# Performance work log

Hardware: AMD Instinct MI355X
Metric: run time of the kernel (lower is better)

Reference implementation:

```python
import jax, jax.numpy as jnp
import numpy as np

N_NODES = 50000
N_EDGES = 800000
IN_DIM, H1, H2 = 512, 128, 64


def setup_inputs() -> dict:
    key = jax.random.key(0)
    k1, k2, k3, k4 = jax.random.split(key, 4)
    x = jax.random.normal(k1, (N_NODES, IN_DIM), dtype=jnp.float32)
    edge_index = jax.random.randint(k2, (2, N_EDGES), 0, N_NODES, dtype=jnp.int64)
    # Glorot-ish scaled weights (PyG GCNConv uses glorot init)
    W1 = jax.random.normal(k3, (IN_DIM, H1), dtype=jnp.float32) * (1.0 / np.sqrt(IN_DIM))
    b1 = jnp.zeros((H1,), dtype=jnp.float32)
    W2 = jax.random.normal(k4, (H1, H2), dtype=jnp.float32) * (1.0 / np.sqrt(H1))
    b2 = jnp.zeros((H2,), dtype=jnp.float32)
    return {"x": x, "edge_index": edge_index, "W1": W1, "b1": b1, "W2": W2, "b2": b2}


def reference(x, edge_index, W1, b1, W2, b2):
    N = x.shape[0]
    # PyG GCNConv default: add self-loops + symmetric normalization
    loop = jnp.arange(N, dtype=edge_index.dtype)
    src = jnp.concatenate([edge_index[0], loop])  # message source j
    dst = jnp.concatenate([edge_index[1], loop])  # aggregation target i
    deg = jax.ops.segment_sum(jnp.ones(src.shape[0], dtype=x.dtype), dst, num_segments=N)
    dinv = jnp.where(deg > 0, jax.lax.rsqrt(deg), 0.0)
    norm = dinv[src] * dinv[dst]  # [E+N]

    def gcn_relu(h, W, b):
        h = h @ W                                   # [N, F_out]
        msg = h[src] * norm[:, None]                # gather + edge scaling
        agg = jax.ops.segment_sum(msg, dst, num_segments=N)  # scatter-add
        return jax.nn.relu(agg + b)

    h = gcn_relu(x, W1, b1)
    return gcn_relu(h, W2, b2)
```

## Files before the change

kernel.cpp:

```cpp
#include <hip/hip_runtime.h>


constexpr int IN_DIM = 512;
constexpr int HD1 = 128;
constexpr int HD2 = 64;

typedef __attribute__((ext_vector_type(8))) short bf16x8;
typedef __attribute__((ext_vector_type(8))) unsigned short u16x8;
typedef __attribute__((ext_vector_type(4))) float f32x4;
typedef unsigned int u32;

__device__ inline unsigned short f2bf(float f) {
    u32 u = __builtin_bit_cast(u32, f);
    return (unsigned short)((u + 0x7fffu + ((u >> 16) & 1u)) >> 16);
}
__device__ inline float bf_lo(u32 v) { return __builtin_bit_cast(float, v << 16); }
__device__ inline float bf_hi(u32 v) { return __builtin_bit_cast(float, v & 0xffff0000u); }

__device__ inline int elem_off(int row, int k) {
    return (row << 6) + (k ^ ((row & 7) << 3));
}
__device__ inline int elem_off128(int row, int k) {
    return (row << 7) + (k ^ ((row & 7) << 3));
}

__global__ __launch_bounds__(256) void k_prep(const int* __restrict__ dst, int E,
                                              int* __restrict__ deg,
                                              int* __restrict__ rank,
                                              const float* __restrict__ W1,
                                              unsigned short* __restrict__ Wt,
                                              const float* __restrict__ W2,
                                              unsigned short* __restrict__ Wt2) {
    int id = blockIdx.x * 256 + threadIdx.x;
    if (id < E) rank[id] = atomicAdd(&deg[dst[id]], 1);
    if (id < IN_DIM * HD1) {
        int n = id >> 9, k = id & 511;
        Wt[id] = f2bf(W1[k * HD1 + n]);
    }
    if (id < HD1 * HD2) {
        int n = id >> 7, k = id & 127;
        Wt2[id] = f2bf(W2[k * HD2 + n]);
    }
}

__global__ __launch_bounds__(256) void k_dinv_bsum(const int* __restrict__ deg, int N,
                                                   float* __restrict__ dinv,
                                                   int* __restrict__ bsum) {
    __shared__ int s[256];
    int t = threadIdx.x;
    int i = blockIdx.x * 256 + t;
    int d = (i < N) ? deg[i] : 0;
    if (i < N) dinv[i] = rsqrtf((float)(d + 1));
    s[t] = d;
    __syncthreads();
    for (int st = 128; st > 0; st >>= 1) {
        if (t < st) s[t] += s[t + st];
        __syncthreads();
    }
    if (t == 0) bsum[blockIdx.x] = s[0];
}

__global__ __launch_bounds__(256) void k_scan_final(const int* __restrict__ deg, int N,
                                                    const int* __restrict__ bsum, int nb,
                                                    int* __restrict__ rowptr) {
    __shared__ int sb[256];
    __shared__ int s[256];
    int t = threadIdx.x;
    sb[t] = (t < nb) ? bsum[t] : 0;
    __syncthreads();
    for (int off = 1; off < 256; off <<= 1) {
        int v = (t >= off) ? sb[t - off] : 0;
        __syncthreads();
        sb[t] += v;
        __syncthreads();
    }
    int base = (blockIdx.x == 0) ? 0 : sb[blockIdx.x - 1];

    int i = blockIdx.x * 256 + t;
    int v = (i < N) ? deg[i] : 0;
    s[t] = v;
    __syncthreads();
    for (int off = 1; off < 256; off <<= 1) {
        int u = (t >= off) ? s[t - off] : 0;
        __syncthreads();
        s[t] += u;
        __syncthreads();
    }
    int incl = s[t] + base;
    if (i < N) rowptr[i] = incl - v;
    if (i == N - 1) rowptr[N] = incl;
}

__global__ __launch_bounds__(256) void k_mega(const float* __restrict__ X,
                                              const unsigned short* __restrict__ Wt,
                                              unsigned short* __restrict__ H, int N,
                                              int gemmBlocks,
                                              const int* __restrict__ src,
                                              const int* __restrict__ dst, int E,
                                              const int* __restrict__ rowptr,
                                              const int* __restrict__ rank,
                                              int* __restrict__ col) {
    __shared__ unsigned short As[128 * 64];
    __shared__ unsigned short Bs[128 * 64];

    if (blockIdx.x >= gemmBlocks) {
        int stride = (gridDim.x - gemmBlocks) * 256;
        for (int e = (blockIdx.x - gemmBlocks) * 256 + threadIdx.x; e < E; e += stride) {
            int d = dst[e];
            col[rowptr[d] + rank[e]] = src[e];
        }
        return;
    }

    const int tid = threadIdx.x;
    const int lane = tid & 63;
    const int wid = tid >> 6;
    const int brow = blockIdx.x * 128;
    const int wr0 = (wid >> 1) * 64;
    const int wc0 = (wid & 1) * 64;
    const bool full = (brow + 128 <= N);

    f32x4 acc[4][4];
#pragma unroll
    for (int i = 0; i < 4; i++)
#pragma unroll
        for (int j = 0; j < 4; j++) acc[i][j] = (f32x4){0.f, 0.f, 0.f, 0.f};

    for (int kt = 0; kt < IN_DIM / 64; kt++) {
        const int k0 = kt * 64;
#pragma unroll
        for (int p = 0; p < 4; p++) {
            int chunk = (wid * 4 + p) * 64 + lane;
            int n = chunk >> 3;
            int kcs = chunk & 7;
            int kc = kcs ^ (n & 7);
            const unsigned short* srcp = &Wt[(size_t)n * IN_DIM + k0 + kc * 8];
            unsigned short* dstp = &Bs[(wid * 4 + p) * 512];
            __builtin_amdgcn_global_load_lds(
                (const __attribute__((address_space(1))) u32*)(const void*)srcp,
                (__attribute__((address_space(3))) u32*)(void*)dstp, 16, 0, 0);
        }
#pragma unroll
        for (int p = 0; p < 4; p++) {
            int chunk = tid + p * 256;
            int r = chunk >> 3;
            int kc = chunk & 7;
            const float* xp = &X[(size_t)(brow + r) * IN_DIM + k0 + kc * 8];
            float4 v0, v1;
            if (full || (brow + r) < N) {
                v0 = *(const float4*)xp;
                v1 = *(const float4*)(xp + 4);
            } else {
                v0 = make_float4(0.f, 0.f, 0.f, 0.f); v1 = v0;
            }
            u16x8 w;
            w[0] = f2bf(v0.x); w[1] = f2bf(v0.y); w[2] = f2bf(v0.z); w[3] = f2bf(v0.w);
            w[4] = f2bf(v1.x); w[5] = f2bf(v1.y); w[6] = f2bf(v1.z); w[7] = f2bf(v1.w);
            *(u16x8*)&As[elem_off(r, kc * 8)] = w;
        }
        __syncthreads();

#pragma unroll
        for (int kk = 0; kk < 2; kk++) {
            const int kel = kk * 32 + (lane >> 4) * 8;
            bf16x8 a[4], b[4];
#pragma unroll
            for (int mi = 0; mi < 4; mi++)
                a[mi] = *(const bf16x8*)&As[elem_off(wr0 + mi * 16 + (lane & 15), kel)];
#pragma unroll
            for (int ni = 0; ni < 4; ni++)
                b[ni] = *(const bf16x8*)&Bs[elem_off(wc0 + ni * 16 + (lane & 15), kel)];
#pragma unroll
            for (int mi = 0; mi < 4; mi++)
#pragma unroll
                for (int ni = 0; ni < 4; ni++)
                    acc[mi][ni] = __builtin_amdgcn_mfma_f32_16x16x32_bf16(
                        a[mi], b[ni], acc[mi][ni], 0, 0, 0);
        }
        __syncthreads();
    }

#pragma unroll
    for (int mi = 0; mi < 4; mi++) {
#pragma unroll
        for (int reg = 0; reg < 4; reg++) {
            int grow = brow + wr0 + mi * 16 + (lane >> 4) * 4 + reg;
            if (grow < N) {
#pragma unroll
                for (int ni = 0; ni < 4; ni++) {
                    int gcol = wc0 + ni * 16 + (lane & 15);
                    H[(size_t)grow * HD1 + gcol] = f2bf(acc[mi][ni][reg]);
                }
            }
        }
    }
}

__global__ __launch_bounds__(256) void k_gather1(const unsigned short* __restrict__ h,
                                                 const int* __restrict__ rowptr,
                                                 const int* __restrict__ col,
                                                 const float* __restrict__ dinv,
                                                 const float* __restrict__ bias,
                                                 unsigned short* __restrict__ out, int N) {
    const int i = (blockIdx.x * 256 + threadIdx.x) >> 6;
    const int lane = threadIdx.x & 63;
    if (i >= N) return;
    const int half = lane >> 5;
    const int c4 = (lane & 31) * 4;
    const float di = dinv[i];
    const unsigned short* hc = h + c4;

    float a0 = 0.f, a1 = 0.f, a2 = 0.f, a3 = 0.f;
    if (half == 0) {
        uint2 sv = *(const uint2*)&hc[(size_t)i * HD1];
        float s = di * di;
        a0 = bf_lo(sv.x) * s; a1 = bf_hi(sv.x) * s;
        a2 = bf_lo(sv.y) * s; a3 = bf_hi(sv.y) * s;
    }
    const int beg = rowptr[i], end = rowptr[i + 1];
    for (int p0 = beg; p0 < end; p0 += 64) {
        int idx = p0 + lane;
        bool okl = idx < end;
        int myj = okl ? col[idx] : i;
        float mydj = okl ? dinv[myj] : 0.f;
        const int cnt8 = (min(64, end - p0) + 7) & ~7;
        uint2 v[4]; float wv[4];
#pragma unroll
        for (int q = 0; q < 4; q++) {
            int e = 2 * q + half;
            int j = __shfl(myj, e);
            wv[q] = __shfl(mydj, e) * di;
            v[q] = *(const uint2*)&hc[(size_t)j * HD1];
        }
        for (int k = 8; k < cnt8; k += 8) {
            uint2 nv[4]; float nw[4];
#pragma unroll
            for (int q = 0; q < 4; q++) {
                int e = k + 2 * q + half;
                int j = __shfl(myj, e);
                nw[q] = __shfl(mydj, e) * di;
                nv[q] = *(const uint2*)&hc[(size_t)j * HD1];
            }
#pragma unroll
            for (int q = 0; q < 4; q++) {
                a0 = fmaf(bf_lo(v[q].x), wv[q], a0);
                a1 = fmaf(bf_hi(v[q].x), wv[q], a1);
                a2 = fmaf(bf_lo(v[q].y), wv[q], a2);
                a3 = fmaf(bf_hi(v[q].y), wv[q], a3);
            }
#pragma unroll
            for (int q = 0; q < 4; q++) { v[q] = nv[q]; wv[q] = nw[q]; }
        }
#pragma unroll
        for (int q = 0; q < 4; q++) {
            a0 = fmaf(bf_lo(v[q].x), wv[q], a0);
            a1 = fmaf(bf_hi(v[q].x), wv[q], a1);
            a2 = fmaf(bf_lo(v[q].y), wv[q], a2);
            a3 = fmaf(bf_hi(v[q].y), wv[q], a3);
        }
    }
    a0 += __shfl_xor(a0, 32);
    a1 += __shfl_xor(a1, 32);
    a2 += __shfl_xor(a2, 32);
    a3 += __shfl_xor(a3, 32);
    if (half == 0) {
        float4 bv = *(const float4*)&bias[c4];
        u32 w0 = (u32)f2bf(fmaxf(a0 + bv.x, 0.f)) | ((u32)f2bf(fmaxf(a1 + bv.y, 0.f)) << 16);
        u32 w1 = (u32)f2bf(fmaxf(a2 + bv.z, 0.f)) | ((u32)f2bf(fmaxf(a3 + bv.w, 0.f)) << 16);
        *(uint2*)&out[(size_t)i * HD1 + c4] = make_uint2(w0, w1);
    }
}

__global__ __launch_bounds__(256) void k_gemm2(const unsigned short* __restrict__ A,
                                               const unsigned short* __restrict__ Wt2,
                                               unsigned short* __restrict__ H, int N) {
    __shared__ unsigned short As[128 * 128];
    __shared__ unsigned short Bs[64 * 128];
    const int tid = threadIdx.x;
    const int lane = tid & 63;
    const int wid = tid >> 6;
    const int brow = blockIdx.x * 128;
    const int wr0 = wid * 32;

#pragma unroll
    for (int p = 0; p < 8; p++) {
        int chunk = (wid * 8 + p) * 64 + lane;
        int r = chunk >> 4;
        int kcs = chunk & 15;
        int kc = kcs ^ (r & 7);
        const unsigned short* src = &A[(size_t)(brow + r) * HD1 + kc * 8];
        unsigned short* dst = &As[(wid * 8 + p) * 512];
        __builtin_amdgcn_global_load_lds(
            (const __attribute__((address_space(1))) u32*)(const void*)src,
            (__attribute__((address_space(3))) u32*)(void*)dst, 16, 0, 0);
    }
#pragma unroll
    for (int p = 0; p < 4; p++) {
        int chunk = (wid * 4 + p) * 64 + lane;
        int c = chunk >> 4;
        int kcs = chunk & 15;
        int kc = kcs ^ (c & 7);
        const unsigned short* src = &Wt2[(size_t)c * HD1 + kc * 8];
        unsigned short* dst = &Bs[(wid * 4 + p) * 512];
        __builtin_amdgcn_global_load_lds(
            (const __attribute__((address_space(1))) u32*)(const void*)src,
            (__attribute__((address_space(3))) u32*)(void*)dst, 16, 0, 0);
    }
    __syncthreads();

    f32x4 acc[2][4];
#pragma unroll
    for (int i = 0; i < 2; i++)
#pragma unroll
        for (int j = 0; j < 4; j++) acc[i][j] = (f32x4){0.f, 0.f, 0.f, 0.f};

#pragma unroll
    for (int kk = 0; kk < 4; kk++) {
        const int kel = kk * 32 + (lane >> 4) * 8;
        bf16x8 a[2], b[4];
#pragma unroll
        for (int mi = 0; mi < 2; mi++)
            a[mi] = *(const bf16x8*)&As[elem_off128(wr0 + mi * 16 + (lane & 15), kel)];
#pragma unroll
        for (int ni = 0; ni < 4; ni++)
            b[ni] = *(const bf16x8*)&Bs[elem_off128(ni * 16 + (lane & 15), kel)];
#pragma unroll
        for (int mi = 0; mi < 2; mi++)
#pragma unroll
            for (int ni = 0; ni < 4; ni++)
                acc[mi][ni] = __builtin_amdgcn_mfma_f32_16x16x32_bf16(
                    a[mi], b[ni], acc[mi][ni], 0, 0, 0);
    }

#pragma unroll
    for (int mi = 0; mi < 2; mi++) {
#pragma unroll
        for (int reg = 0; reg < 4; reg++) {
            int grow = brow + wr0 + mi * 16 + (lane >> 4) * 4 + reg;
            if (grow < N) {
#pragma unroll
                for (int ni = 0; ni < 4; ni++) {
                    int gcol = ni * 16 + (lane & 15);
                    H[(size_t)grow * HD2 + gcol] = f2bf(acc[mi][ni][reg]);
                }
            }
        }
    }
}

__global__ __launch_bounds__(256) void k_gather2(const unsigned short* __restrict__ h,
                                                 const int* __restrict__ rowptr,
                                                 const int* __restrict__ col,
                                                 const float* __restrict__ dinv,
                                                 const float* __restrict__ bias,
                                                 float* __restrict__ out, int N) {
    const int i = (blockIdx.x * 256 + threadIdx.x) >> 6;
    const int lane = threadIdx.x & 63;
    if (i >= N) return;
    const int half = lane >> 5;
    const int c2 = (lane & 31) * 2;
    const float di = dinv[i];
    const unsigned short* hc = h + c2;

    float a0 = 0.f, a1 = 0.f;
    if (half == 0) {
        u32 sv = *(const u32*)&hc[(size_t)i * HD2];
        float s = di * di;
        a0 = bf_lo(sv) * s; a1 = bf_hi(sv) * s;
    }
    const int beg = rowptr[i], end = rowptr[i + 1];
    for (int p0 = beg; p0 < end; p0 += 64) {
        int idx = p0 + lane;
        bool okl = idx < end;
        int myj = okl ? col[idx] : i;
        float mydj = okl ? dinv[myj] : 0.f;
        const int cnt8 = (min(64, end - p0) + 7) & ~7;
        u32 v[4]; float wv[4];
#pragma unroll
        for (int q = 0; q < 4; q++) {
            int e = 2 * q + half;
            int j = __shfl(myj, e);
            wv[q] = __shfl(mydj, e) * di;
            v[q] = *(const u32*)&hc[(size_t)j * HD2];
        }
        for (int k = 8; k < cnt8; k += 8) {
            u32 nv[4]; float nw[4];
#pragma unroll
            for (int q = 0; q < 4; q++) {
                int e = k + 2 * q + half;
                int j = __shfl(myj, e);
                nw[q] = __shfl(mydj, e) * di;
                nv[q] = *(const u32*)&hc[(size_t)j * HD2];
            }
#pragma unroll
            for (int q = 0; q < 4; q++) {
                a0 = fmaf(bf_lo(v[q]), wv[q], a0);
                a1 = fmaf(bf_hi(v[q]), wv[q], a1);
            }
#pragma unroll
            for (int q = 0; q < 4; q++) { v[q] = nv[q]; wv[q] = nw[q]; }
        }
#pragma unroll
        for (int q = 0; q < 4; q++) {
            a0 = fmaf(bf_lo(v[q]), wv[q], a0);
            a1 = fmaf(bf_hi(v[q]), wv[q], a1);
        }
    }
    a0 += __shfl_xor(a0, 32);
    a1 += __shfl_xor(a1, 32);
    if (half == 0) {
        float2 bv = *(const float2*)&bias[c2];
        float2 r = make_float2(fmaxf(a0 + bv.x, 0.f), fmaxf(a1 + bv.y, 0.f));
        *(float2*)&out[(size_t)i * HD2 + c2] = r;
    }
}

extern "C" void kernel_launch(void* const* d_in, const int* in_sizes, int n_in,
                              void* d_out, int out_size, void* d_ws, size_t ws_size,
                              hipStream_t stream) {
    const float* x  = (const float*)d_in[0];
    const int*   ei = (const int*)d_in[1];
    const float* W1 = (const float*)d_in[2];
    const float* b1 = (const float*)d_in[3];
    const float* W2 = (const float*)d_in[4];
    const float* b2 = (const float*)d_in[5];
    float* out = (float*)d_out;

    const int N = in_sizes[0] / IN_DIM;
    const int E = in_sizes[1] / 2;
    const int* src = ei;
    const int* dst = ei + E;

    char* w = (char*)d_ws;
    size_t off = 0;
    auto alloc = [&](size_t bytes) -> void* {
        void* p = w + off;
        off = (off + bytes + 255) & ~(size_t)255;
        return p;
    };
    int*   deg    = (int*)alloc((size_t)N * 4);
    int*   rank   = (int*)alloc((size_t)E * 4);
    int*   rowptr = (int*)alloc((size_t)(N + 1) * 4);
    int*   bsum   = (int*)alloc(1024 * 4);
    int*   col    = (int*)alloc((size_t)E * 4);
    float* dinv   = (float*)alloc((size_t)N * 4);
    unsigned short* Wt  = (unsigned short*)alloc((size_t)IN_DIM * HD1 * 2);
    unsigned short* Wt2 = (unsigned short*)alloc((size_t)HD2 * HD1 * 2);
    unsigned short* h1  = (unsigned short*)alloc((size_t)N * HD1 * 2);
    unsigned short* agg1= (unsigned short*)alloc((size_t)(N + 128) * HD1 * 2);
    unsigned short* h2  = h1;

    hipMemsetAsync(deg, 0, (size_t)N * 4, stream);

    const int nb = (N + 255) / 256;
    const int eb = (E + 255) / 256;
    const int gemmBlocks = (N + 127) / 128;
    const int fillBlocks = 512;

    k_prep<<<eb, 256, 0, stream>>>(dst, E, deg, rank, W1, Wt, W2, Wt2);
    k_dinv_bsum<<<nb, 256, 0, stream>>>(deg, N, dinv, bsum);
    k_scan_final<<<nb, 256, 0, stream>>>(deg, N, bsum, nb, rowptr);

    k_mega<<<gemmBlocks + fillBlocks, 256, 0, stream>>>(
        x, Wt, h1, N, gemmBlocks, src, dst, E, rowptr, rank, col);

    k_gather1<<<(N * 64 + 255) / 256, 256, 0, stream>>>(h1, rowptr, col, dinv, b1, agg1, N);
    k_gemm2<<<(N + 127) / 128, 256, 0, stream>>>(agg1, Wt2, h2, N);
    k_gather2<<<(N * 64 + 255) / 256, 256, 0, stream>>>(h2, rowptr, col, dinv, b2, out, N);
}
```

Before: 147.3 us.

## Load X directly into registers and double-buffer weight tiles in fused GEMM

The first GEMM stops staging X through shared memory. Each wave now loads its fp32 X rows straight from global memory, converts them to bf16 in registers and feeds them to MFMA. The weight tiles are double-buffered in LDS, with the next tile's async load issued before computing the current one, which removes one barrier per k-step. The CSR fill path batches four edges per thread with nontemporal stores, and the number of fill blocks doubles. The tradeoff is that each X element is now read by both column waves, so uncoalesced global traffic rises and there is more register pressure.

```diff
diff --git a/kernel.cpp b/kernel.cpp
--- a/kernel.cpp
+++ b/kernel.cpp
@@ -91,6 +91,22 @@
     if (i == N - 1) rowptr[N] = incl;
 }
 
+__device__ inline void issue_b_tile(const unsigned short* __restrict__ Wt, int k0,
+                                    unsigned short* bs, int wid, int lane) {
+#pragma unroll
+    for (int p = 0; p < 4; p++) {
+        int chunk = (wid * 4 + p) * 64 + lane;
+        int n = chunk >> 3;
+        int kcs = chunk & 7;
+        int kc = kcs ^ (n & 7);
+        const unsigned short* srcp = &Wt[(size_t)n * IN_DIM + k0 + kc * 8];
+        unsigned short* dstp = bs + (wid * 4 + p) * 512;
+        __builtin_amdgcn_global_load_lds(
+            (const __attribute__((address_space(1))) u32*)(const void*)srcp,
+            (__attribute__((address_space(3))) u32*)(void*)dstp, 16, 0, 0);
+    }
+}
+
 __global__ __launch_bounds__(256) void k_mega(const float* __restrict__ X,
                                               const unsigned short* __restrict__ Wt,
                                               unsigned short* __restrict__ H, int N,
@@ -100,12 +116,28 @@
                                               const int* __restrict__ rowptr,
                                               const int* __restrict__ rank,
                                               int* __restrict__ col) {
-    __shared__ unsigned short As[128 * 64];
-    __shared__ unsigned short Bs[128 * 64];
+    __shared__ unsigned short Bs[2][128 * 64];
 
     if (blockIdx.x >= gemmBlocks) {
-        int stride = (gridDim.x - gemmBlocks) * 256;
-        for (int e = (blockIdx.x - gemmBlocks) * 256 + threadIdx.x; e < E; e += stride) {
+        const int T = (gridDim.x - gemmBlocks) * 256;
+        const int e0 = (blockIdx.x - gemmBlocks) * 256 + threadIdx.x;
+        const int e1 = e0 + T, e2 = e1 + T, e3 = e2 + T;
+        const bool v0 = e0 < E, v1 = e1 < E, v2 = e2 < E, v3 = e3 < E;
+        int d0, d1, d2, d3, r0, r1, r2, r3, s0, s1, s2, s3;
+        if (v0) { d0 = dst[e0]; r0 = rank[e0]; s0 = src[e0]; }
+        if (v1) { d1 = dst[e1]; r1 = rank[e1]; s1 = src[e1]; }
+        if (v2) { d2 = dst[e2]; r2 = rank[e2]; s2 = src[e2]; }
+        if (v3) { d3 = dst[e3]; r3 = rank[e3]; s3 = src[e3]; }
+        int p0, p1, p2, p3;
+        if (v0) p0 = rowptr[d0] + r0;
+        if (v1) p1 = rowptr[d1] + r1;
+        if (v2) p2 = rowptr[d2] + r2;
+        if (v3) p3 = rowptr[d3] + r3;
+        if (v0) __builtin_nontemporal_store(s0, &col[p0]);
+        if (v1) __builtin_nontemporal_store(s1, &col[p1]);
+        if (v2) __builtin_nontemporal_store(s2, &col[p2]);
+        if (v3) __builtin_nontemporal_store(s3, &col[p3]);
+        for (int e = e0 + 4 * T; e < E; e += T) {
             int d = dst[e];
             col[rowptr[d] + rank[e]] = src[e];
         }
@@ -126,50 +158,36 @@
 #pragma unroll
         for (int j = 0; j < 4; j++) acc[i][j] = (f32x4){0.f, 0.f, 0.f, 0.f};
 
+    issue_b_tile(Wt, 0, &Bs[0][0], wid, lane);
+
     for (int kt = 0; kt < IN_DIM / 64; kt++) {
-        const int k0 = kt * 64;
-#pragma unroll
-        for (int p = 0; p < 4; p++) {
-            int chunk = (wid * 4 + p) * 64 + lane;
-            int n = chunk >> 3;
-            int kcs = chunk & 7;
-            int kc = kcs ^ (n & 7);
-            const unsigned short* srcp = &Wt[(size_t)n * IN_DIM + k0 + kc * 8];
-            unsigned short* dstp = &Bs[(wid * 4 + p) * 512];
-            __builtin_amdgcn_global_load_lds(
-                (const __attribute__((address_space(1))) u32*)(const void*)srcp,
-                (__attribute__((address_space(3))) u32*)(void*)dstp, 16, 0, 0);
-        }
-#pragma unroll
-        for (int p = 0; p < 4; p++) {
-            int chunk = tid + p * 256;
-            int r = chunk >> 3;
-            int kc = chunk & 7;
-            const float* xp = &X[(size_t)(brow + r) * IN_DIM + k0 + kc * 8];
-            float4 v0, v1;
-            if (full || (brow + r) < N) {
-                v0 = *(const float4*)xp;
-                v1 = *(const float4*)(xp + 4);
-            } else {
-                v0 = make_float4(0.f, 0.f, 0.f, 0.f); v1 = v0;
-            }
-            u16x8 w;
-            w[0] = f2bf(v0.x); w[1] = f2bf(v0.y); w[2] = f2bf(v0.z); w[3] = f2bf(v0.w);
-            w[4] = f2bf(v1.x); w[5] = f2bf(v1.y); w[6] = f2bf(v1.z); w[7] = f2bf(v1.w);
-            *(u16x8*)&As[elem_off(r, kc * 8)] = w;
-        }
-        __syncthreads();
+        const int cur = kt & 1;
+        __syncthreads();
+        if (kt + 1 < IN_DIM / 64)
+            issue_b_tile(Wt, (kt + 1) * 64, &Bs[cur ^ 1][0], wid, lane);
 
 #pragma unroll
         for (int kk = 0; kk < 2; kk++) {
             const int kel = kk * 32 + (lane >> 4) * 8;
+            const int kg = kt * 64 + kel;
             bf16x8 a[4], b[4];
 #pragma unroll
-            for (int mi = 0; mi < 4; mi++)
-                a[mi] = *(const bf16x8*)&As[elem_off(wr0 + mi * 16 + (lane & 15), kel)];
+            for (int mi = 0; mi < 4; mi++) {
+                const int grow = brow + wr0 + mi * 16 + (lane & 15);
+                float4 v0 = make_float4(0.f, 0.f, 0.f, 0.f), v1 = v0;
+                if (full || grow < N) {
+                    const float* xp = &X[(size_t)grow * IN_DIM + kg];
+                    v0 = *(const float4*)xp;
+                    v1 = *(const float4*)(xp + 4);
+                }
+                u16x8 w;
+                w[0] = f2bf(v0.x); w[1] = f2bf(v0.y); w[2] = f2bf(v0.z); w[3] = f2bf(v0.w);
+                w[4] = f2bf(v1.x); w[5] = f2bf(v1.y); w[6] = f2bf(v1.z); w[7] = f2bf(v1.w);
+                a[mi] = __builtin_bit_cast(bf16x8, w);
+            }
 #pragma unroll
             for (int ni = 0; ni < 4; ni++)
-                b[ni] = *(const bf16x8*)&Bs[elem_off(wc0 + ni * 16 + (lane & 15), kel)];
+                b[ni] = *(const bf16x8*)&Bs[cur][elem_off(wc0 + ni * 16 + (lane & 15), kel)];
 #pragma unroll
             for (int mi = 0; mi < 4; mi++)
 #pragma unroll
@@ -177,7 +195,6 @@
                     acc[mi][ni] = __builtin_amdgcn_mfma_f32_16x16x32_bf16(
                         a[mi], b[ni], acc[mi][ni], 0, 0, 0);
         }
-        __syncthreads();
     }
 
 #pragma unroll
@@ -455,7 +472,7 @@
     const int nb = (N + 255) / 256;
     const int eb = (E + 255) / 256;
     const int gemmBlocks = (N + 127) / 128;
-    const int fillBlocks = 512;
+    const int fillBlocks = 1024;
 
     k_prep<<<eb, 256, 0, stream>>>(dst, E, deg, rank, W1, Wt, W2, Wt2);
     k_dinv_bsum<<<nb, 256, 0, stream>>>(deg, N, dinv, bsum);
```

Result: slower. 158.4 us (+7.5%).

## Split fused GEMM+CSR-fill kernel; rewrite GEMM1 as LDS-free register-direct MFMA

Applied to the files above, without the earlier changes.

The combined kernel, which ran the first-layer GEMM alongside the CSR column fill, is split into a separate k_fill launch and a new k_gemm1. The new GEMM uses no shared memory. Each wave computes a 16x128 tile, loading X rows straight into registers (converted to bf16) and reading W fragments from global memory, with no barriers. This removes the LDS staging and syncthreads overhead and allows higher occupancy, at the cost of redundant global/L2 reads of W across waves and an extra launch that no longer overlaps the fill with the GEMM.

```diff
diff --git a/kernel.cpp b/kernel.cpp
--- a/kernel.cpp
+++ b/kernel.cpp
@@ -17,9 +17,6 @@
 __device__ inline float bf_lo(u32 v) { return __builtin_bit_cast(float, v << 16); }
 __device__ inline float bf_hi(u32 v) { return __builtin_bit_cast(float, v & 0xffff0000u); }
 
-__device__ inline int elem_off(int row, int k) {
-    return (row << 6) + (k ^ ((row & 7) << 3));
-}
 __device__ inline int elem_off128(int row, int k) {
     return (row << 7) + (k ^ ((row & 7) << 3));
 }
@@ -91,107 +88,62 @@
     if (i == N - 1) rowptr[N] = incl;
 }
 
-__global__ __launch_bounds__(256) void k_mega(const float* __restrict__ X,
-                                              const unsigned short* __restrict__ Wt,
-                                              unsigned short* __restrict__ H, int N,
-                                              int gemmBlocks,
-                                              const int* __restrict__ src,
+__global__ __launch_bounds__(256) void k_fill(const int* __restrict__ src,
                                               const int* __restrict__ dst, int E,
                                               const int* __restrict__ rowptr,
                                               const int* __restrict__ rank,
                                               int* __restrict__ col) {
-    __shared__ unsigned short As[128 * 64];
-    __shared__ unsigned short Bs[128 * 64];
-
-    if (blockIdx.x >= gemmBlocks) {
-        int stride = (gridDim.x - gemmBlocks) * 256;
-        for (int e = (blockIdx.x - gemmBlocks) * 256 + threadIdx.x; e < E; e += stride) {
-            int d = dst[e];
-            col[rowptr[d] + rank[e]] = src[e];
-        }
-        return;
-    }
-
-    const int tid = threadIdx.x;
-    const int lane = tid & 63;
-    const int wid = tid >> 6;
-    const int brow = blockIdx.x * 128;
-    const int wr0 = (wid >> 1) * 64;
-    const int wc0 = (wid & 1) * 64;
-    const bool full = (brow + 128 <= N);
-
-    f32x4 acc[4][4];
-#pragma unroll
-    for (int i = 0; i < 4; i++)
-#pragma unroll
-        for (int j = 0; j < 4; j++) acc[i][j] = (f32x4){0.f, 0.f, 0.f, 0.f};
-
-    for (int kt = 0; kt < IN_DIM / 64; kt++) {
-        const int k0 = kt * 64;
-#pragma unroll
-        for (int p = 0; p < 4; p++) {
-            int chunk = (wid * 4 + p) * 64 + lane;
-            int n = chunk >> 3;
-            int kcs = chunk & 7;
-            int kc = kcs ^ (n & 7);
-            const unsigned short* srcp = &Wt[(size_t)n * IN_DIM + k0 + kc * 8];
-            unsigned short* dstp = &Bs[(wid * 4 + p) * 512];
-            __builtin_amdgcn_global_load_lds(
-                (const __attribute__((address_space(1))) u32*)(const void*)srcp,
-                (__attribute__((address_space(3))) u32*)(void*)dstp, 16, 0, 0);
-        }
-#pragma unroll
-        for (int p = 0; p < 4; p++) {
-            int chunk = tid + p * 256;
-            int r = chunk >> 3;
-            int kc = chunk & 7;
-            const float* xp = &X[(size_t)(brow + r) * IN_DIM + k0 + kc * 8];
-            float4 v0, v1;
-            if (full || (brow + r) < N) {
-                v0 = *(const float4*)xp;
-                v1 = *(const float4*)(xp + 4);
-            } else {
-                v0 = make_float4(0.f, 0.f, 0.f, 0.f); v1 = v0;
-            }
-            u16x8 w;
-            w[0] = f2bf(v0.x); w[1] = f2bf(v0.y); w[2] = f2bf(v0.z); w[3] = f2bf(v0.w);
-            w[4] = f2bf(v1.x); w[5] = f2bf(v1.y); w[6] = f2bf(v1.z); w[7] = f2bf(v1.w);
-            *(u16x8*)&As[elem_off(r, kc * 8)] = w;
-        }
-        __syncthreads();
-
-#pragma unroll
-        for (int kk = 0; kk < 2; kk++) {
-            const int kel = kk * 32 + (lane >> 4) * 8;
-            bf16x8 a[4], b[4];
-#pragma unroll
-            for (int mi = 0; mi < 4; mi++)
-                a[mi] = *(const bf16x8*)&As[elem_off(wr0 + mi * 16 + (lane & 15), kel)];
-#pragma unroll
-            for (int ni = 0; ni < 4; ni++)
-                b[ni] = *(const bf16x8*)&Bs[elem_off(wc0 + ni * 16 + (lane & 15), kel)];
-#pragma unroll
-            for (int mi = 0; mi < 4; mi++)
-#pragma unroll
-                for (int ni = 0; ni < 4; ni++)
-                    acc[mi][ni] = __builtin_amdgcn_mfma_f32_16x16x32_bf16(
-                        a[mi], b[ni], acc[mi][ni], 0, 0, 0);
-        }
-        __syncthreads();
-    }
-
-#pragma unroll
-    for (int mi = 0; mi < 4; mi++) {
-#pragma unroll
-        for (int reg = 0; reg < 4; reg++) {
-            int grow = brow + wr0 + mi * 16 + (lane >> 4) * 4 + reg;
-            if (grow < N) {
-#pragma unroll
-                for (int ni = 0; ni < 4; ni++) {
-                    int gcol = wc0 + ni * 16 + (lane & 15);
-                    H[(size_t)grow * HD1 + gcol] = f2bf(acc[mi][ni][reg]);
-                }
-            }
+    int e = blockIdx.x * 256 + threadIdx.x;
+    if (e < E) {
+        int d = dst[e];
+        col[rowptr[d] + rank[e]] = src[e];
+    }
+}
+
+__global__ __launch_bounds__(256) void k_gemm1(const float* __restrict__ X,
+                                               const unsigned short* __restrict__ Wt,
+                                               unsigned short* __restrict__ H, int N) {
+    const int lane = threadIdx.x & 63;
+    const int wid = threadIdx.x >> 6;
+    const int r15 = lane & 15;
+    const int k8 = (lane >> 4) * 8;
+    const int row = blockIdx.x * 64 + wid * 16 + r15;
+    const bool rok = row < N;
+    const float* xrow = &X[(size_t)row * IN_DIM];
+
+    f32x4 acc[8];
+#pragma unroll
+    for (int j = 0; j < 8; j++) acc[j] = (f32x4){0.f, 0.f, 0.f, 0.f};
+
+#pragma unroll 2
+    for (int kt = 0; kt < 16; kt++) {
+        const int kg = kt * 32 + k8;
+        bf16x8 b[8];
+#pragma unroll
+        for (int ni = 0; ni < 8; ni++)
+            b[ni] = *(const bf16x8*)&Wt[(size_t)(ni * 16 + r15) * IN_DIM + kg];
+        float4 v0 = make_float4(0.f, 0.f, 0.f, 0.f), v1 = v0;
+        if (rok) {
+            v0 = *(const float4*)&xrow[kg];
+            v1 = *(const float4*)&xrow[kg + 4];
+        }
+        u16x8 w;
+        w[0] = f2bf(v0.x); w[1] = f2bf(v0.y); w[2] = f2bf(v0.z); w[3] = f2bf(v0.w);
+        w[4] = f2bf(v1.x); w[5] = f2bf(v1.y); w[6] = f2bf(v1.z); w[7] = f2bf(v1.w);
+        bf16x8 a = __builtin_bit_cast(bf16x8, w);
+#pragma unroll
+        for (int ni = 0; ni < 8; ni++)
+            acc[ni] = __builtin_amdgcn_mfma_f32_16x16x32_bf16(a, b[ni], acc[ni], 0, 0, 0);
+    }
+
+    const int brow = blockIdx.x * 64 + wid * 16;
+#pragma unroll
+    for (int reg = 0; reg < 4; reg++) {
+        int grow = brow + (lane >> 4) * 4 + reg;
+        if (grow < N) {
+#pragma unroll
+            for (int ni = 0; ni < 8; ni++)
+                H[(size_t)grow * HD1 + ni * 16 + r15] = f2bf(acc[ni][reg]);
         }
     }
 }
@@ -454,16 +406,13 @@
 
     const int nb = (N + 255) / 256;
     const int eb = (E + 255) / 256;
-    const int gemmBlocks = (N + 127) / 128;
-    const int fillBlocks = 512;
 
     k_prep<<<eb, 256, 0, stream>>>(dst, E, deg, rank, W1, Wt, W2, Wt2);
     k_dinv_bsum<<<nb, 256, 0, stream>>>(deg, N, dinv, bsum);
     k_scan_final<<<nb, 256, 0, stream>>>(deg, N, bsum, nb, rowptr);
-
-    k_mega<<<gemmBlocks + fillBlocks, 256, 0, stream>>>(
-        x, Wt, h1, N, gemmBlocks, src, dst, E, rowptr, rank, col);
-
+    k_fill<<<eb, 256, 0, stream>>>(src, dst, E, rowptr, rank, col);
+
+    k_gemm1<<<(N + 63) / 64, 256, 0, stream>>>(x, Wt, h1, N);
     k_gather1<<<(N * 64 + 255) / 256, 256, 0, stream>>>(h1, rowptr, col, dinv, b1, agg1, N);
     k_gemm2<<<(N + 127) / 128, 256, 0, stream>>>(agg1, Wt2, h2, N);
     k_gather2<<<(N * 64 + 255) / 256, 256, 0, stream>>>(h2, rowptr, col, dinv, b2, out, N);
```

Result: slower. 200.1 us (+35.8%).
